# Kernel optimization log

Measured on AMD Instinct MI355X. Metric: run time of the kernel, lower is better.

Reference implementation:

```python
import jax, jax.numpy as jnp
import numpy as np

EPS_NORM = 1e-5
EPS_L2 = 1e-12
SCALE_VALUE = 50.0
FROM_VALUE = 0.4
VALUE_INTERVAL = 0.5


def mvn(x):
    # mean-variance norm per (b, c) over spatial dims; torch .var() is unbiased
    mean = jnp.mean(x, axis=(2, 3), keepdims=True)
    var = jnp.var(x, axis=(2, 3), keepdims=True, ddof=1)
    return (x - mean) / jnp.sqrt(var + EPS_NORM)


def conv1x1(x, W, b):
    # x: [b,c,h,w], W: [out,in], b: [out]
    return jnp.einsum('bchw,oc->bohw', x, W) + b[None, :, None, None]


def setup_inputs() -> dict:
    key = jax.random.key(0)
    ks = jax.random.split(key, 12)
    B, C, Hs, Ws = 4, 512, 64, 64
    HW = Hs * Ws  # 4096 == spatial_dims
    HID = HW // 16
    sc = 1.0 / np.sqrt(C)
    inp = {
        'content': jax.random.normal(ks[0], (B, C, Hs, Ws), jnp.float32),
        'style': jax.random.normal(ks[1], (B, C, Hs, Ws), jnp.float32),
        'Wf': jax.random.normal(ks[2], (C, C), jnp.float32) * sc,
        'bf': jnp.zeros((C,), jnp.float32),
        'Wg': jax.random.normal(ks[3], (C, C), jnp.float32) * sc,
        'bg': jnp.zeros((C,), jnp.float32),
        'Wh': jax.random.normal(ks[4], (C, C), jnp.float32) * sc,
        'bh': jnp.zeros((C,), jnp.float32),
        'Wout': jax.random.normal(ks[5], (C, C), jnp.float32) * sc,
        'bout': jnp.zeros((C,), jnp.float32),
        'W1': jax.random.normal(ks[6], (HID, HW), jnp.float32) * (1.0 / np.sqrt(HW)),
        'b1': jnp.zeros((HID,), jnp.float32),
        'W2': jax.random.normal(ks[7], (1, HID), jnp.float32) * (1.0 / np.sqrt(HID)),
        'b2': jnp.zeros((1,), jnp.float32),
    }
    return inp


def reference(content, style, Wf, bf, Wg, bg, Wh, bh, Wout, bout, W1, b1, W2, b2):
    B, C, H, W = content.shape
    HW = H * W

    Fq = conv1x1(mvn(content), Wf, bf).reshape(B, C, HW)   # query feats
    Gk = conv1x1(mvn(style), Wg, bg).reshape(B, C, HW)      # key feats
    Hv = conv1x1(style, Wh, bh).reshape(B, C, HW)           # value feats

    # affinity matrix: channel-L2-normalized cosine similarity [B, HW_c, HW_s]
    cf = content.reshape(B, C, HW)
    sf = style.reshape(B, C, HW)
    cf = cf / jnp.maximum(jnp.linalg.norm(cf, axis=1, keepdims=True), EPS_L2)
    sf = sf / jnp.maximum(jnp.linalg.norm(sf, axis=1, keepdims=True), EPS_L2)
    A = jnp.einsum('bck,bcl->bkl', cf, sf)

    # attention scores + softmax over style positions
    S = jax.nn.softmax(jnp.einsum('bck,bcl->bkl', Fq, Gk), axis=-1)

    # AEAModule: per-content-pixel adaptive clamp from affinity rows
    hmid = jnp.einsum('bkl,ol->bko', A, W1) + b1            # [B, HW, HID]
    hmid = jax.nn.leaky_relu(hmid, 0.2)
    psi = jax.nn.sigmoid(jnp.einsum('bko,po->bkp', hmid, W2) + b2)  # [B, HW, 1]
    clamp_value = psi * VALUE_INTERVAL + FROM_VALUE
    Sg = jax.nn.sigmoid(SCALE_VALUE * (S - clamp_value))    # gated attention

    # O = H @ Sg^T : [B, C, HW_c]
    O = jnp.einsum('bcl,bkl->bck', Hv, Sg).reshape(B, C, H, W)
    O = conv1x1(O, Wout, bout) + content
    return O
```

## Files before the change

### kernel.cpp

```cpp
#include <hip/hip_runtime.h>

typedef unsigned short u16;
typedef __attribute__((ext_vector_type(8))) short short8;
typedef __attribute__((ext_vector_type(4))) float f32x4;

static constexpr int Bn  = 4;
static constexpr int C   = 512;
static constexpr int HW  = 4096;
static constexpr int HID = 256;

__device__ __forceinline__ float bf2f(u16 u){
  union { unsigned int i; float f; } x; x.i = ((unsigned int)u) << 16; return x.f;
}
__device__ __forceinline__ u16 f2bf(float f){
  union { float f; unsigned int i; } x; x.f = f;
  return (u16)((x.i + 0x7fffu + ((x.i >> 16) & 1u)) >> 16);
}
__device__ __forceinline__ void gld16(const u16* g, u16* l){
  __builtin_amdgcn_global_load_lds((const __attribute__((address_space(1))) void*)g,
                                   (__attribute__((address_space(3))) void*)l, 16, 0, 0);
}

template<bool SPLIT>
__device__ __forceinline__ void mfma_core(const u16* __restrict__ Ah, const u16* __restrict__ Al, int pA,
                                          const u16* __restrict__ Bh, const u16* __restrict__ Bl, int pB,
                                          int K, u16* lds, f32x4 (&acc)[4][4]){
  const int tid  = threadIdx.x;
  const int lane = tid & 63, wave = tid >> 6;
  const int fr = lane & 15, kq = lane >> 4;
  const int wm = (wave & 1) * 64, wn = (wave >> 1) * 64;
  u16* As  = lds;
  u16* Bs  = lds + 4096;
  u16* As2 = SPLIT ? lds + 8192  : nullptr;
  u16* Bs2 = SPLIT ? lds + 12288 : nullptr;
  const int srow = wave*32 + (lane >> 2);
  const int sq   = (lane & 3) * 8;
  const size_t ga = (size_t)srow * pA + sq;
  const size_t gb = (size_t)srow * pB + sq;
  const int ldsc = wave * 1024;

  for (int k0 = 0; k0 < K; k0 += 32){
    __syncthreads();
    #pragma unroll
    for (int i = 0; i < 2; ++i){
      gld16(Ah + ga + (size_t)i*16*pA + k0, As + ldsc + i*512);
      gld16(Bh + gb + (size_t)i*16*pB + k0, Bs + ldsc + i*512);
      if (SPLIT){
        gld16(Al + ga + (size_t)i*16*pA + k0, As2 + ldsc + i*512);
        gld16(Bl + gb + (size_t)i*16*pB + k0, Bs2 + ldsc + i*512);
      }
    }
    __syncthreads();
    short8 a[4], b[4];
    #pragma unroll
    for (int i = 0; i < 4; ++i){
      a[i] = *(const short8*)&As[(wm + i*16 + fr)*32 + kq*8];
      b[i] = *(const short8*)&Bs[(wn + i*16 + fr)*32 + kq*8];
    }
    #pragma unroll
    for (int i = 0; i < 4; ++i)
      #pragma unroll
      for (int j = 0; j < 4; ++j)
        acc[i][j] = __builtin_amdgcn_mfma_f32_16x16x32_bf16(a[i], b[j], acc[i][j], 0, 0, 0);
    if (SPLIT){
      short8 a2[4], b2[4];
      #pragma unroll
      for (int i = 0; i < 4; ++i){
        a2[i] = *(const short8*)&As2[(wm + i*16 + fr)*32 + kq*8];
        b2[i] = *(const short8*)&Bs2[(wn + i*16 + fr)*32 + kq*8];
      }
      #pragma unroll
      for (int i = 0; i < 4; ++i)
        #pragma unroll
        for (int j = 0; j < 4; ++j){
          acc[i][j] = __builtin_amdgcn_mfma_f32_16x16x32_bf16(a[i],  b2[j], acc[i][j], 0, 0, 0);
          acc[i][j] = __builtin_amdgcn_mfma_f32_16x16x32_bf16(a2[i], b[j],  acc[i][j], 0, 0, 0);
        }
    }
  }
}

struct TileCtx { int wm, wn, cn, rq; };
__device__ __forceinline__ TileCtx tctx(){
  TileCtx t;
  const int wave = threadIdx.x >> 6, lane = threadIdx.x & 63;
  t.wm = blockIdx.y * 128 + (wave & 1) * 64;
  t.wn = blockIdx.x * 128 + (wave >> 1) * 64;
  t.cn = lane & 15; t.rq = (lane >> 4) * 4;
  return t;
}
#define ACC_ZERO(acc) { _Pragma("unroll") for (int i=0;i<4;++i) _Pragma("unroll") for (int j=0;j<4;++j) _Pragma("unroll") for (int r=0;r<4;++r) acc[i][j][r]=0.f; }

__global__ __launch_bounds__(256) void g_conv_split2(const u16* __restrict__ A0h, const u16* __restrict__ A0l,
                                                     const u16* __restrict__ A1h, const u16* __restrict__ A1l,
                                                     const u16* __restrict__ B0h, const u16* __restrict__ B0l,
                                                     const u16* __restrict__ B1h, const u16* __restrict__ B1l,
                                                     const float* __restrict__ bias0, const float* __restrict__ bias1,
                                                     u16* __restrict__ O0h, u16* __restrict__ O0l,
                                                     u16* __restrict__ O1h, u16* __restrict__ O1l,
                                                     size_t bsA, size_t bsO){
  __shared__ u16 lds[16384];
  const int zb = blockIdx.z, b = zb >> 1, z = zb & 1;
  const u16* Ah = (z ? A1h : A0h) + (size_t)b*bsA;  const u16* Al = (z ? A1l : A0l) + (size_t)b*bsA;
  const u16* Bh = z ? B1h : B0h;  const u16* Bl = z ? B1l : B0l;
  const float* bias = z ? bias1 : bias0;
  u16* Ohi = (z ? O1h : O0h) + (size_t)b*bsO;  u16* Olo = (z ? O1l : O0l) + (size_t)b*bsO;
  TileCtx t = tctx();
  f32x4 acc[4][4]; ACC_ZERO(acc);
  mfma_core<true>(Ah + (size_t)blockIdx.y*128*C, Al + (size_t)blockIdx.y*128*C, C,
                  Bh + (size_t)blockIdx.x*128*C, Bl + (size_t)blockIdx.x*128*C, C, C, lds, acc);
  #pragma unroll
  for (int fm = 0; fm < 4; ++fm)
    #pragma unroll
    for (int fn = 0; fn < 4; ++fn)
      #pragma unroll
      for (int r = 0; r < 4; ++r){
        int gm = t.wm + fm*16 + t.rq + r;
        int gn = t.wn + fn*16 + t.cn;
        float v = acc[fm][fn][r] + bias[gn];
        u16 h = f2bf(v);
        Ohi[(size_t)gm*C + gn] = h;
        Olo[(size_t)gm*C + gn] = f2bf(v - bf2f(h));
      }
}

__global__ __launch_bounds__(256) void g_gemm_split_f32(const u16* __restrict__ Ah, const u16* __restrict__ Al, int pA,
                                                        const u16* __restrict__ Bh, const u16* __restrict__ Bl, int pB,
                                                        int K, float* __restrict__ O, int pO,
                                                        size_t bsA, size_t bsB, size_t bsO){
  __shared__ u16 lds[16384];
  const int b = blockIdx.z;
  TileCtx t = tctx();
  f32x4 acc[4][4]; ACC_ZERO(acc);
  mfma_core<true>(Ah + (size_t)b*bsA + (size_t)blockIdx.y*128*pA,
                  Al + (size_t)b*bsA + (size_t)blockIdx.y*128*pA, pA,
                  Bh + (size_t)b*bsB + (size_t)blockIdx.x*128*pB,
                  Bl + (size_t)b*bsB + (size_t)blockIdx.x*128*pB, pB, K, lds, acc);
  float* Ob = O + (size_t)b*bsO;
  #pragma unroll
  for (int fm = 0; fm < 4; ++fm)
    #pragma unroll
    for (int fn = 0; fn < 4; ++fn)
      #pragma unroll
      for (int r = 0; r < 4; ++r)
        Ob[(size_t)(t.wm + fm*16 + t.rq + r)*pO + t.wn + fn*16 + t.cn] = acc[fm][fn][r];
}

__global__ __launch_bounds__(256) void g_gemm_biasm_bf16(const u16* __restrict__ A, int pA,
                                                         const u16* __restrict__ B, int pB,
                                                         int K, const float* __restrict__ bias,
                                                         u16* __restrict__ O, int pO,
                                                         size_t bsB, size_t bsO){
  __shared__ u16 lds[8192];
  const int b = blockIdx.z;
  TileCtx t = tctx();
  f32x4 acc[4][4]; ACC_ZERO(acc);
  mfma_core<false>(A + (size_t)blockIdx.y*128*pA, nullptr, pA,
                   B + (size_t)b*bsB + (size_t)blockIdx.x*128*pB, nullptr, pB, K, lds, acc);
  u16* Ob = O + (size_t)b*bsO;
  #pragma unroll
  for (int fm = 0; fm < 4; ++fm)
    #pragma unroll
    for (int fn = 0; fn < 4; ++fn)
      #pragma unroll
      for (int r = 0; r < 4; ++r){
        int gm = t.wm + fm*16 + t.rq + r;
        Ob[(size_t)gm*pO + t.wn + fn*16 + t.cn] = f2bf(acc[fm][fn][r] + bias[gm]);
      }
}

__global__ __launch_bounds__(256) void g_gemm_plain_bf16(const u16* __restrict__ A, int pA,
                                                         const u16* __restrict__ B, int pB,
                                                         int K, u16* __restrict__ O, int pO,
                                                         size_t bsA, size_t bsB, size_t bsO){
  __shared__ u16 lds[8192];
  const int b = blockIdx.z;
  TileCtx t = tctx();
  f32x4 acc[4][4]; ACC_ZERO(acc);
  mfma_core<false>(A + (size_t)b*bsA + (size_t)blockIdx.y*128*pA, nullptr, pA,
                   B + (size_t)b*bsB + (size_t)blockIdx.x*128*pB, nullptr, pB, K, lds, acc);
  u16* Ob = O + (size_t)b*bsO;
  #pragma unroll
  for (int fm = 0; fm < 4; ++fm)
    #pragma unroll
    for (int fn = 0; fn < 4; ++fn)
      #pragma unroll
      for (int r = 0; r < 4; ++r){
        int gm = t.wm + fm*16 + t.rq + r;
        Ob[(size_t)gm*pO + t.wn + fn*16 + t.cn] = f2bf(acc[fm][fn][r]);
      }
}

__global__ __launch_bounds__(256) void g_gemm_partial(const u16* __restrict__ A, int pA,
                                                      const u16* __restrict__ B, int pB,
                                                      int Kper, float* __restrict__ O, int pO,
                                                      size_t sliceStride, int slices,
                                                      size_t bsB, size_t bsO){
  __shared__ u16 lds[8192];
  const int zz = blockIdx.z;
  const int b = zz / slices, sl = zz - b*slices;
  TileCtx t = tctx();
  const int koff = sl * Kper;
  f32x4 acc[4][4]; ACC_ZERO(acc);
  mfma_core<false>(A + (size_t)blockIdx.y*128*pA + koff, nullptr, pA,
                   B + (size_t)b*bsB + (size_t)blockIdx.x*128*pB + koff, nullptr, pB, Kper, lds, acc);
  float* Oz = O + (size_t)b*bsO + (size_t)sl * sliceStride;
  #pragma unroll
  for (int fm = 0; fm < 4; ++fm)
    #pragma unroll
    for (int fn = 0; fn < 4; ++fn)
      #pragma unroll
      for (int r = 0; r < 4; ++r)
        Oz[(size_t)(t.wm + fm*16 + t.rq + r)*pO + t.wn + fn*16 + t.cn] = acc[fm][fn][r];
}

__global__ __launch_bounds__(256) void k_reduce(const float* __restrict__ in, size_t sliceStride,
                                                int S, u16* __restrict__ out,
                                                size_t bsIn, size_t bsOut){
  const int b = blockIdx.y;
  const float* inb = in + (size_t)b*bsIn;
  u16* outb = out + (size_t)b*bsOut;
  const size_t i4 = ((size_t)blockIdx.x*256 + threadIdx.x) * 4;
  float4 s = *(const float4*)&inb[i4];
  for (int z = 1; z < S; ++z){
    float4 v = *(const float4*)&inb[(size_t)z*sliceStride + i4];
    s.x += v.x; s.y += v.y; s.z += v.z; s.w += v.w;
  }
  u16 r0 = f2bf(s.x), r1 = f2bf(s.y), r2 = f2bf(s.z), r3 = f2bf(s.w);
  uint2 uo; uo.x = (unsigned)r0 | ((unsigned)r1 << 16);
  uo.y = (unsigned)r2 | ((unsigned)r3 << 16);
  *(uint2*)&outb[i4] = uo;
}

__global__ __launch_bounds__(256) void g_gemm_outconv(const u16* __restrict__ A, int pA,
                                                      const u16* __restrict__ B, int pB,
                                                      int K, const float* __restrict__ bias,
                                                      const float* __restrict__ res,
                                                      float* __restrict__ O,
                                                      size_t bsB, size_t bsRes, size_t bsO){
  __shared__ u16 lds[8192];
  const int b = blockIdx.z;
  TileCtx t = tctx();
  f32x4 acc[4][4]; ACC_ZERO(acc);
  mfma_core<false>(A + (size_t)blockIdx.y*128*pA, nullptr, pA,
                   B + (size_t)b*bsB + (size_t)blockIdx.x*128*pB, nullptr, pB, K, lds, acc);
  const float* resb = res + (size_t)b*bsRes;
  float* Ob = O + (size_t)b*bsO;
  #pragma unroll
  for (int fm = 0; fm < 4; ++fm)
    #pragma unroll
    for (int fn = 0; fn < 4; ++fn)
      #pragma unroll
      for (int r = 0; r < 4; ++r){
        int gm = t.wm + fm*16 + t.rq + r;
        int gn = t.wn + fn*16 + t.cn;
        Ob[(size_t)gm*HW + gn] = acc[fm][fn][r] + bias[gm] + resb[(size_t)gm*HW + gn];
      }
}

__global__ __launch_bounds__(256) void g_gemm_hmid(const u16* __restrict__ A, int pA,
                                                   const u16* __restrict__ B, int pB,
                                                   int K, const float* __restrict__ inc,
                                                   const float* __restrict__ b1,
                                                   float* __restrict__ O,
                                                   size_t bsA, size_t bsP, size_t bsInc, size_t bsO){
  __shared__ u16 lds[8192];
  const int b = blockIdx.z;
  TileCtx t = tctx();
  f32x4 acc[4][4]; ACC_ZERO(acc);
  mfma_core<false>(A + (size_t)b*bsA + (size_t)blockIdx.y*128*pA, nullptr, pA,
                   B + (size_t)b*bsP + (size_t)blockIdx.x*128*pB, nullptr, pB, K, lds, acc);
  const float* incb = inc + (size_t)b*bsInc;
  float* Ob = O + (size_t)b*bsO;
  #pragma unroll
  for (int fm = 0; fm < 4; ++fm)
    #pragma unroll
    for (int fn = 0; fn < 4; ++fn)
      #pragma unroll
      for (int r = 0; r < 4; ++r){
        int gm = t.wm + fm*16 + t.rq + r;
        int gn = t.wn + fn*16 + t.cn;
        float h = acc[fm][fn][r] * incb[gm] + b1[gn];
        Ob[(size_t)gm*HID + gn] = (h > 0.f) ? h : 0.2f*h;
      }
}

__global__ __launch_bounds__(256) void k_stats(const float* __restrict__ content,
                                               const float* __restrict__ style,
                                               float2* __restrict__ statsC,
                                               float2* __restrict__ statsS){
  const int bc = blockIdx.x;
  const float* X = (blockIdx.y == 0 ? content : style) + (size_t)bc * HW;
  float s = 0.f, sq = 0.f;
  for (int i = threadIdx.x; i < HW; i += 256){ float v = X[i]; s += v; sq += v*v; }
  __shared__ float rs[256], rq[256];
  rs[threadIdx.x] = s; rq[threadIdx.x] = sq; __syncthreads();
  for (int o = 128; o > 0; o >>= 1){
    if (threadIdx.x < o){ rs[threadIdx.x] += rs[threadIdx.x+o]; rq[threadIdx.x] += rq[threadIdx.x+o]; }
    __syncthreads();
  }
  if (threadIdx.x == 0){
    float mean = rs[0] / (float)HW;
    float var  = (rq[0] - rs[0]*mean) / (float)(HW - 1);
    (blockIdx.y == 0 ? statsC : statsS)[bc] = make_float2(mean, rsqrtf(var + 1e-5f));
  }
}

__global__ __launch_bounds__(256) void k_pixnorm(const float* __restrict__ content,
                                                 const float* __restrict__ style,
                                                 float* __restrict__ inc,
                                                 float* __restrict__ ins){
  const int b = blockIdx.y;
  const int k = blockIdx.x * 256 + threadIdx.x;
  const float* X = (blockIdx.z == 0 ? content : style) + (size_t)b * C * HW + k;
  float acc = 0.f;
  for (int c = 0; c < C; ++c){ float v = X[(size_t)c * HW]; acc += v*v; }
  (blockIdx.z == 0 ? inc : ins)[b*HW + k] = 1.f / fmaxf(sqrtf(acc), 1e-12f);
}

__global__ __launch_bounds__(256) void k_prep2(const float* __restrict__ Xc,
                                               const float* __restrict__ Xs,
                                               const float2* __restrict__ stC,
                                               const float2* __restrict__ stS,
                                               u16* __restrict__ ThiC, u16* __restrict__ TloC, u16* __restrict__ TrawC,
                                               u16* __restrict__ ThiS, u16* __restrict__ TloS, u16* __restrict__ TrawS,
                                               size_t bsX, size_t bsT, int bsSt){
  const int zb = blockIdx.z, b = zb >> 1, z = zb & 1;
  const float* X = (z ? Xs : Xc) + (size_t)b*bsX;
  const float2* stats = (z ? stS : stC) + (size_t)b*bsSt;
  u16* Thi = (z ? ThiS : ThiC) + (size_t)b*bsT;
  u16* Tlo = (z ? TloS : TloC) + (size_t)b*bsT;
  u16* Traw = (z ? TrawS : TrawC) + (size_t)b*bsT;
  __shared__ float tile[64][65];
  __shared__ float2 st[64];
  const int k0 = blockIdx.x*64, c0 = blockIdx.y*64;
  const int t = threadIdx.x;
  if (t < 64) st[t] = stats[c0 + t];
  const int j4 = (t & 15) * 4, i0 = t >> 4;
  for (int r = 0; r < 4; ++r){
    int i = i0 + r*16;
    float4 v = *(const float4*)&X[(size_t)(c0+i)*HW + k0 + j4];
    tile[i][j4+0] = v.x; tile[i][j4+1] = v.y; tile[i][j4+2] = v.z; tile[i][j4+3] = v.w;
  }
  __syncthreads();
  const int kk = t >> 2, cc = (t & 3) * 16;
  u16 h[16], l[16], rw[16];
  #pragma unroll
  for (int q = 0; q < 16; ++q){
    float x = tile[cc+q][kk];
    float2 s = st[cc+q];
    rw[q] = f2bf(x);
    float v = (x - s.x) * s.y;
    h[q] = f2bf(v);
    l[q] = f2bf(v - bf2f(h[q]));
  }
  size_t o = (size_t)(k0+kk)*C + c0 + cc;
  #pragma unroll
  for (int q = 0; q < 16; ++q){ Thi[o+q] = h[q]; Tlo[o+q] = l[q]; Traw[o+q] = rw[q]; }
}

__global__ __launch_bounds__(256) void k_scaleS(const float* __restrict__ style,
                                                const float* __restrict__ ins,
                                                u16* __restrict__ out,
                                                size_t bsS, size_t bsIns, size_t bsO){
  const int b = blockIdx.y;
  const size_t idx = ((size_t)blockIdx.x*256 + threadIdx.x) * 4;
  const int l = (int)(idx % HW);
  float4 v = *(const float4*)&style[(size_t)b*bsS + idx];
  float4 s = *(const float4*)&ins[(size_t)b*bsIns + l];
  u16* ob = out + (size_t)b*bsO;
  ob[idx+0] = f2bf(v.x*s.x); ob[idx+1] = f2bf(v.y*s.y);
  ob[idx+2] = f2bf(v.z*s.z); ob[idx+3] = f2bf(v.w*s.w);
}

__global__ __launch_bounds__(256) void k_wprep(const float* __restrict__ Wf, const float* __restrict__ Wg,
                                               const float* __restrict__ Wh, const float* __restrict__ Wo,
                                               const float* __restrict__ W1,
                                               u16* __restrict__ Wfh, u16* __restrict__ Wfl,
                                               u16* __restrict__ Wgh, u16* __restrict__ Wgl,
                                               u16* __restrict__ Whb, u16* __restrict__ Wob,
                                               u16* __restrict__ W1b){
  const int idx = (blockIdx.x*256 + threadIdx.x) * 4;
  const int mode = blockIdx.y;
  const int nsmall = C*C;
  if (mode == 4){
    float4 v = *(const float4*)&W1[idx];
    W1b[idx+0]=f2bf(v.x); W1b[idx+1]=f2bf(v.y); W1b[idx+2]=f2bf(v.z); W1b[idx+3]=f2bf(v.w);
    return;
  }
  if (idx >= nsmall) return;
  const float* src = (mode==0)?Wf:(mode==1)?Wg:(mode==2)?Wh:Wo;
  float4 v = *(const float4*)&src[idx];
  float vv[4] = {v.x, v.y, v.z, v.w};
  if (mode <= 1){
    u16* oh = (mode==0)?Wfh:Wgh;  u16* ol = (mode==0)?Wfl:Wgl;
    #pragma unroll
    for (int q = 0; q < 4; ++q){
      u16 hh = f2bf(vv[q]);
      oh[idx+q] = hh; ol[idx+q] = f2bf(vv[q] - bf2f(hh));
    }
  } else {
    u16* ob = (mode==2)?Whb:Wob;
    #pragma unroll
    for (int q = 0; q < 4; ++q) ob[idx+q] = f2bf(vv[q]);
  }
}

__global__ __launch_bounds__(256) void k_psi(const float* __restrict__ hmid,
                                             const float* __restrict__ W2,
                                             const float* __restrict__ b2,
                                             float* __restrict__ clampv,
                                             size_t bsH, size_t bsC){
  const int k = blockIdx.x, tid = threadIdx.x, b = blockIdx.y;
  __shared__ float red[256];
  red[tid] = hmid[(size_t)b*bsH + (size_t)k*HID + tid] * W2[tid];
  __syncthreads();
  for (int o = 128; o > 0; o >>= 1){
    if (tid < o) red[tid] += red[tid+o];
    __syncthreads();
  }
  if (tid == 0){
    float psi = 1.f/(1.f + expf(-(red[0] + b2[0])));
    clampv[(size_t)b*bsC + k] = psi*0.5f + 0.4f;
  }
}

__global__ __launch_bounds__(256) void k_softgate(float* __restrict__ T2,
                                                  const float* __restrict__ clampv,
                                                  size_t bsT, size_t bsC){
  const int k = blockIdx.x, tid = threadIdx.x, b = blockIdx.y;
  float* row = &T2[(size_t)b*bsT + (size_t)k*HW];
  float vals[16];
  float mx = -3.4e38f;
  #pragma unroll
  for (int i = 0; i < 16; ++i){ vals[i] = row[tid + i*256]; mx = fmaxf(mx, vals[i]); }
  __shared__ float red[256];
  red[tid] = mx; __syncthreads();
  for (int o = 128; o > 0; o >>= 1){
    if (tid < o) red[tid] = fmaxf(red[tid], red[tid+o]);
    __syncthreads();
  }
  mx = red[0]; __syncthreads();
  float s = 0.f;
  #pragma unroll
  for (int i = 0; i < 16; ++i){ vals[i] = expf(vals[i] - mx); s += vals[i]; }
  red[tid] = s; __syncthreads();
  for (int o = 128; o > 0; o >>= 1){
    if (tid < o) red[tid] += red[tid+o];
    __syncthreads();
  }
  const float inv = 1.f / red[0];
  const float cv = clampv[(size_t)b*bsC + k];
  u16* Sg = (u16*)row;
  #pragma unroll
  for (int i = 0; i < 16; ++i){
    float sg = 1.f/(1.f + expf(-50.f*(vals[i]*inv - cv)));
    Sg[tid + i*256] = f2bf(sg);
  }
}

extern "C" void kernel_launch(void* const* d_in, const int* in_sizes, int n_in,
                              void* d_out, int out_size, void* d_ws, size_t ws_size,
                              hipStream_t stream){
  const float* content = (const float*)d_in[0];
  const float* style   = (const float*)d_in[1];
  const float* Wf   = (const float*)d_in[2];  const float* bfv  = (const float*)d_in[3];
  const float* Wg   = (const float*)d_in[4];  const float* bg   = (const float*)d_in[5];
  const float* Wh   = (const float*)d_in[6];  const float* bh   = (const float*)d_in[7];
  const float* Wo   = (const float*)d_in[8];  const float* bout = (const float*)d_in[9];
  const float* W1   = (const float*)d_in[10]; const float* b1   = (const float*)d_in[11];
  const float* W2   = (const float*)d_in[12]; const float* b2   = (const float*)d_in[13];
  float* out = (float*)d_out;
  (void)in_sizes; (void)n_in; (void)out_size;

  char* ws = (char*)d_ws;
  size_t off = 0;
  auto alloc = [&](size_t bytes)->void*{
    void* p = (void*)(ws + off);
    off += (bytes + 255) & ~(size_t)255;
    return p;
  };
  float2* statsC = (float2*)alloc((size_t)Bn*C*sizeof(float2));
  float2* statsS = (float2*)alloc((size_t)Bn*C*sizeof(float2));
  float*  inc    = (float*) alloc((size_t)Bn*HW*sizeof(float));
  float*  ins    = (float*) alloc((size_t)Bn*HW*sizeof(float));
  float*  clampv = (float*) alloc((size_t)Bn*HW*sizeof(float));
  u16* Wfh = (u16*)alloc((size_t)C*C*2), *Wfl = (u16*)alloc((size_t)C*C*2);
  u16* Wgh = (u16*)alloc((size_t)C*C*2), *Wgl = (u16*)alloc((size_t)C*C*2);
  u16* Whb = (u16*)alloc((size_t)C*C*2), *Wob = (u16*)alloc((size_t)C*C*2);
  u16* W1b = (u16*)alloc((size_t)HID*HW*2);
  const size_t commonEnd = off;

  const size_t TPB = (size_t)HW*C;
  const size_t XB  = (size_t)C*HW;
  const size_t SLB = (size_t)Bn*TPB*2;

  k_stats  <<<dim3(Bn*C, 2),       256, 0, stream>>>(content, style, statsC, statsS);
  k_pixnorm<<<dim3(HW/256, Bn, 2), 256, 0, stream>>>(content, style, inc, ins);
  k_wprep  <<<dim3(HID*HW/1024, 5),256, 0, stream>>>(Wf, Wg, Wh, Wo, W1,
                                                     Wfh, Wfl, Wgh, Wgl, Whb, Wob, W1b);

  auto runPrep = [&](char* R, u16* bFqTh, u16* bFqTl, u16* bGkTh, u16* bGkTl,
                     u16* bHvb, u16* bPT){
    u16* bXcTh = (u16*)(R + 0*SLB);
    u16* bXcTl = (u16*)(R + 1*SLB);
    u16* bXsTh = (u16*)(R + 2*SLB);
    u16* bXsTl = (u16*)(R + 3*SLB);
    u16* bCrT  = (u16*)(R + 4*SLB);
    u16* bSrT  = (u16*)(R + 5*SLB);
    u16* bstS  = (u16*)(R + 6*SLB);
    float* bPpart = (float*)(R + 0*SLB);
    float* bhmid  = (float*)(R + 1*SLB);
    k_prep2 <<<dim3(HW/64, C/64, 2*Bn), 256, 0, stream>>>(content, style, statsC, statsS,
                                                          bXcTh, bXcTl, bCrT, bXsTh, bXsTl, bSrT,
                                                          XB, TPB, C);
    k_scaleS<<<dim3(C*HW/1024, Bn), 256, 0, stream>>>(style, ins, bstS, XB, HW, TPB);
    g_conv_split2<<<dim3(C/128, HW/128, 2*Bn), 256, 0, stream>>>(
        bXcTh, bXcTl, bXsTh, bXsTl, Wfh, Wfl, Wgh, Wgl, bfv, bg,
        bFqTh, bFqTl, bGkTh, bGkTl, TPB, TPB);
    g_gemm_biasm_bf16<<<dim3(HW/128, C/128, Bn), 256, 0, stream>>>(Whb, C, bSrT, C, C, bh,
                                                                   bHvb, HW, TPB, TPB);
    g_gemm_partial<<<dim3(C/128, HID/128, Bn*8), 256, 0, stream>>>(W1b, HW, bstS, HW, HW/8,
                                                                   bPpart, C, (size_t)HID*C, 8,
                                                                   TPB, (size_t)8*HID*C);
    k_reduce<<<dim3(HID*C/1024, Bn), 256, 0, stream>>>(bPpart, (size_t)HID*C, 8, bPT,
                                                       (size_t)8*HID*C, (size_t)HID*C);
    g_gemm_hmid<<<dim3(HID/128, HW/128, Bn), 256, 0, stream>>>(bCrT, C, bPT, C, C, inc, b1, bhmid,
                                                               TPB, (size_t)HID*C, HW, (size_t)HW*HID);
    k_psi<<<dim3(HW, Bn), 256, 0, stream>>>(bhmid, W2, b2, clampv, (size_t)HW*HID, HW);
  };

  {
    size_t o = commonEnd;
    auto al = [&](size_t bytes)->void*{ void* p = (void*)(ws + o); o += (bytes + 255) & ~(size_t)255; return p; };
    u16* bFqTh = (u16*)al(SLB), *bFqTl = (u16*)al(SLB);
    u16* bGkTh = (u16*)al(SLB), *bGkTl = (u16*)al(SLB);
    u16* bHvb  = (u16*)al(SLB);
    u16* bPT   = (u16*)al((size_t)Bn*HID*C*2);
    u16* bO1T  = (u16*)al(SLB);
    char* R    = (char*)al((size_t)Bn*HW*HW*4);
    if (o <= ws_size){
      runPrep(R, bFqTh, bFqTl, bGkTh, bGkTl, bHvb, bPT);
      float* bT2 = (float*)R;
      g_gemm_split_f32<<<dim3(HW/128, HW/128, Bn), 256, 0, stream>>>(bFqTh, bFqTl, C, bGkTh, bGkTl, C,
                                                                     C, bT2, HW,
                                                                     TPB, TPB, (size_t)HW*HW);
      k_softgate<<<dim3(HW, Bn), 256, 0, stream>>>(bT2, clampv, (size_t)HW*HW, HW);
      g_gemm_plain_bf16<<<dim3(C/128, HW/128, Bn), 256, 0, stream>>>((const u16*)bT2, 2*HW, bHvb, HW,
                                                                     HW, bO1T, C,
                                                                     (size_t)HW*HW*2, TPB, TPB);
      g_gemm_outconv<<<dim3(HW/128, C/128, Bn), 256, 0, stream>>>(Wob, C, bO1T, C, C, bout, content, out,
                                                                  TPB, XB, XB);
      return;
    }
  }

  {
    size_t o = commonEnd;
    auto al = [&](size_t bytes)->void*{ void* p = (void*)(ws + o); o += (bytes + 255) & ~(size_t)255; return p; };
    u16* bFqTh = (u16*)al(SLB), *bFqTl = (u16*)al(SLB);
    u16* bGkTh = (u16*)al(SLB), *bGkTl = (u16*)al(SLB);
    u16* bHvb  = (u16*)al(SLB);
    u16* bPT   = (u16*)al((size_t)Bn*HID*C*2);
    char* R    = (char*)al(7*SLB);
    if (o <= ws_size){
      runPrep(R, bFqTh, bFqTl, bGkTh, bGkTl, bHvb, bPT);
      float* T2s   = (float*)(R + 0*SLB);
      float* Opart = (float*)(R + 4*SLB);
      u16*   O1Ts  = (u16*)  (R + 6*SLB);
      for (int b = 0; b < Bn; ++b){
        g_gemm_split_f32<<<dim3(HW/128, HW/128), 256, 0, stream>>>(
            bFqTh + (size_t)b*TPB, bFqTl + (size_t)b*TPB, C,
            bGkTh + (size_t)b*TPB, bGkTl + (size_t)b*TPB, C, C, T2s, HW, 0, 0, 0);
        k_softgate<<<dim3(HW), 256, 0, stream>>>(T2s, clampv + (size_t)b*HW, 0, 0);
        g_gemm_partial<<<dim3(C/128, HW/128, 4), 256, 0, stream>>>(
            (const u16*)T2s, 2*HW, bHvb + (size_t)b*TPB, HW, 1024,
            Opart, C, (size_t)HW*C, 4, 0, 0);
        k_reduce<<<dim3(HW*C/1024), 256, 0, stream>>>(Opart, (size_t)HW*C, 4, O1Ts, 0, 0);
        g_gemm_outconv<<<dim3(HW/128, C/128), 256, 0, stream>>>(Wob, C, O1Ts, C, C, bout,
            content + (size_t)b*XB, out + (size_t)b*XB, 0, 0, 0);
      }
      return;
    }
  }

  off = commonEnd;
  u16* XcTh = (u16*)alloc((size_t)HW*C*2), *XcTl = (u16*)alloc((size_t)HW*C*2);
  u16* CrT  = (u16*)alloc((size_t)HW*C*2);
  u16* XsTh = (u16*)alloc((size_t)HW*C*2), *XsTl = (u16*)alloc((size_t)HW*C*2);
  u16* SrT  = (u16*)alloc((size_t)HW*C*2);
  u16* stS  = (u16*)alloc((size_t)C*HW*2);
  u16* FqTh = (u16*)alloc((size_t)HW*C*2), *FqTl = (u16*)alloc((size_t)HW*C*2);
  u16* GkTh = (u16*)alloc((size_t)HW*C*2), *GkTl = (u16*)alloc((size_t)HW*C*2);
  u16* Hvb  = (u16*)alloc((size_t)C*HW*2);
  u16* O1T  = (u16*)alloc((size_t)HW*C*2);
  u16* PT   = (u16*)alloc((size_t)HID*C*2);
  float* hmid  = (float*)alloc((size_t)HW*HID*sizeof(float));
  float* Ppart = (float*)alloc((size_t)16*HID*C*sizeof(float));
  float* Opart = (float*)alloc((size_t)4*HW*C*sizeof(float));
  float* T2    = (float*)alloc((size_t)HW*HW*sizeof(float));

  for (int b = 0; b < Bn; ++b){
    const float* cb = content + (size_t)b*C*HW;
    const float* sb = style   + (size_t)b*C*HW;
    const float* incb = inc + (size_t)b*HW;
    const float* insb = ins + (size_t)b*HW;
    float* clb = clampv + (size_t)b*HW;

    k_prep2 <<<dim3(HW/64, C/64, 2), 256, 0, stream>>>(cb, sb, statsC + (size_t)b*C, statsS + (size_t)b*C,
                                                       XcTh, XcTl, CrT, XsTh, XsTl, SrT, 0, 0, 0);
    k_scaleS<<<dim3(C*HW/1024),   256, 0, stream>>>(sb, insb, stS, 0, 0, 0);
    g_conv_split2<<<dim3(C/128, HW/128, 2), 256, 0, stream>>>(
        XcTh, XcTl, XsTh, XsTl, Wfh, Wfl, Wgh, Wgl, bfv, bg,
        FqTh, FqTl, GkTh, GkTl, 0, 0);
    g_gemm_biasm_bf16<<<dim3(HW/128, C/128), 256, 0, stream>>>(Whb, C, SrT, C, C, bh, Hvb, HW, 0, 0);
    g_gemm_partial<<<dim3(C/128, HID/128, 16), 256, 0, stream>>>(W1b, HW, stS, HW, 256,
                                                                 Ppart, C, (size_t)HID*C, 16, 0, 0);
    k_reduce<<<dim3(HID*C/1024), 256, 0, stream>>>(Ppart, (size_t)HID*C, 16, PT, 0, 0);
    g_gemm_hmid<<<dim3(HID/128, HW/128), 256, 0, stream>>>(CrT, C, PT, C, C, incb, b1, hmid, 0, 0, 0, 0);
    k_psi<<<dim3(HW), 256, 0, stream>>>(hmid, W2, b2, clb, 0, 0);
    g_gemm_split_f32<<<dim3(HW/128, HW/128), 256, 0, stream>>>(FqTh, FqTl, C, GkTh, GkTl, C, C, T2, HW, 0, 0, 0);
    k_softgate<<<dim3(HW), 256, 0, stream>>>(T2, clb, 0, 0);
    g_gemm_partial<<<dim3(C/128, HW/128, 4), 256, 0, stream>>>((const u16*)T2, 2*HW, Hvb, HW, 1024,
                                                               Opart, C, (size_t)HW*C, 4, 0, 0);
    k_reduce<<<dim3(HW*C/1024), 256, 0, stream>>>(Opart, (size_t)HW*C, 4, O1T, 0, 0);
    g_gemm_outconv<<<dim3(HW/128, C/128), 256, 0, stream>>>(Wob, C, O1T, C, C, bout, cb,
                                                            out + (size_t)b*C*HW, 0, 0, 0);
  }
}
```

Before: 914.6 us.

## Double-buffer LDS staging in MFMA GEMM core and fuse style scaling into prep

The shared GEMM core now uses two LDS buffers: global-to-LDS loads for the next K-slice are issued before computing the current one, with explicit vmcnt waits and barriers in place of the previous load-then-compute sequence. This aims to hide global load latency behind MFMA work across all GEMM kernels. LDS allocations double, which may lower occupancy for the split kernels (64KB per block). The separate k_scaleS kernel is also folded into k_prep2, which writes the scaled style output while it already holds the style tile, saving a launch and a second read of style.

```diff
diff --git a/kernel.cpp b/kernel.cpp
--- a/kernel.cpp
+++ b/kernel.cpp
@@ -29,45 +29,44 @@
   const int lane = tid & 63, wave = tid >> 6;
   const int fr = lane & 15, kq = lane >> 4;
   const int wm = (wave & 1) * 64, wn = (wave >> 1) * 64;
-  u16* As  = lds;
-  u16* Bs  = lds + 4096;
-  u16* As2 = SPLIT ? lds + 8192  : nullptr;
-  u16* Bs2 = SPLIT ? lds + 12288 : nullptr;
+  constexpr int HB = SPLIT ? 16384 : 8192;
   const int srow = wave*32 + (lane >> 2);
   const int sq   = (lane & 3) * 8;
   const size_t ga = (size_t)srow * pA + sq;
   const size_t gb = (size_t)srow * pB + sq;
   const int ldsc = wave * 1024;
 
-  for (int k0 = 0; k0 < K; k0 += 32){
-    __syncthreads();
+  auto stage = [&](int buf, int k0){
+    u16* L = lds + buf*HB;
     #pragma unroll
     for (int i = 0; i < 2; ++i){
-      gld16(Ah + ga + (size_t)i*16*pA + k0, As + ldsc + i*512);
-      gld16(Bh + gb + (size_t)i*16*pB + k0, Bs + ldsc + i*512);
-      if (SPLIT){
-        gld16(Al + ga + (size_t)i*16*pA + k0, As2 + ldsc + i*512);
-        gld16(Bl + gb + (size_t)i*16*pB + k0, Bs2 + ldsc + i*512);
+      gld16(Ah + ga + (size_t)i*16*pA + k0, L + ldsc + i*512);
+      gld16(Bh + gb + (size_t)i*16*pB + k0, L + 4096 + ldsc + i*512);
+      if constexpr (SPLIT){
+        gld16(Al + ga + (size_t)i*16*pA + k0, L + 8192  + ldsc + i*512);
+        gld16(Bl + gb + (size_t)i*16*pB + k0, L + 12288 + ldsc + i*512);
       }
     }
-    __syncthreads();
+  };
+  auto compute = [&](int buf){
+    u16* L = lds + buf*HB;
     short8 a[4], b[4];
     #pragma unroll
     for (int i = 0; i < 4; ++i){
-      a[i] = *(const short8*)&As[(wm + i*16 + fr)*32 + kq*8];
-      b[i] = *(const short8*)&Bs[(wn + i*16 + fr)*32 + kq*8];
+      a[i] = *(const short8*)&L[(wm + i*16 + fr)*32 + kq*8];
+      b[i] = *(const short8*)&L[4096 + (wn + i*16 + fr)*32 + kq*8];
     }
     #pragma unroll
     for (int i = 0; i < 4; ++i)
       #pragma unroll
       for (int j = 0; j < 4; ++j)
         acc[i][j] = __builtin_amdgcn_mfma_f32_16x16x32_bf16(a[i], b[j], acc[i][j], 0, 0, 0);
-    if (SPLIT){
+    if constexpr (SPLIT){
       short8 a2[4], b2[4];
       #pragma unroll
       for (int i = 0; i < 4; ++i){
-        a2[i] = *(const short8*)&As2[(wm + i*16 + fr)*32 + kq*8];
-        b2[i] = *(const short8*)&Bs2[(wn + i*16 + fr)*32 + kq*8];
+        a2[i] = *(const short8*)&L[8192  + (wm + i*16 + fr)*32 + kq*8];
+        b2[i] = *(const short8*)&L[12288 + (wn + i*16 + fr)*32 + kq*8];
       }
       #pragma unroll
       for (int i = 0; i < 4; ++i)
@@ -77,7 +76,22 @@
           acc[i][j] = __builtin_amdgcn_mfma_f32_16x16x32_bf16(a2[i], b[j],  acc[i][j], 0, 0, 0);
         }
     }
-  }
+  };
+
+  stage(0, 0);
+  int cur = 0;
+  for (int k0 = 32; k0 < K; k0 += 32){
+    stage(cur ^ 1, k0);
+    if constexpr (SPLIT) asm volatile("s_waitcnt vmcnt(8)" ::: "memory");
+    else                 asm volatile("s_waitcnt vmcnt(4)" ::: "memory");
+    __builtin_amdgcn_s_barrier();
+    compute(cur);
+    __builtin_amdgcn_s_barrier();
+    cur ^= 1;
+  }
+  asm volatile("s_waitcnt vmcnt(0)" ::: "memory");
+  __builtin_amdgcn_s_barrier();
+  compute(cur);
 }
 
 struct TileCtx { int wm, wn, cn, rq; };
@@ -99,7 +113,7 @@
                                                      u16* __restrict__ O0h, u16* __restrict__ O0l,
                                                      u16* __restrict__ O1h, u16* __restrict__ O1l,
                                                      size_t bsA, size_t bsO){
-  __shared__ u16 lds[16384];
+  __shared__ u16 lds[32768];
   const int zb = blockIdx.z, b = zb >> 1, z = zb & 1;
   const u16* Ah = (z ? A1h : A0h) + (size_t)b*bsA;  const u16* Al = (z ? A1l : A0l) + (size_t)b*bsA;
   const u16* Bh = z ? B1h : B0h;  const u16* Bl = z ? B1l : B0l;
@@ -128,7 +142,7 @@
                                                         const u16* __restrict__ Bh, const u16* __restrict__ Bl, int pB,
                                                         int K, float* __restrict__ O, int pO,
                                                         size_t bsA, size_t bsB, size_t bsO){
-  __shared__ u16 lds[16384];
+  __shared__ u16 lds[32768];
   const int b = blockIdx.z;
   TileCtx t = tctx();
   f32x4 acc[4][4]; ACC_ZERO(acc);
@@ -151,7 +165,7 @@
                                                          int K, const float* __restrict__ bias,
                                                          u16* __restrict__ O, int pO,
                                                          size_t bsB, size_t bsO){
-  __shared__ u16 lds[8192];
+  __shared__ u16 lds[16384];
   const int b = blockIdx.z;
   TileCtx t = tctx();
   f32x4 acc[4][4]; ACC_ZERO(acc);
@@ -173,7 +187,7 @@
                                                          const u16* __restrict__ B, int pB,
                                                          int K, u16* __restrict__ O, int pO,
                                                          size_t bsA, size_t bsB, size_t bsO){
-  __shared__ u16 lds[8192];
+  __shared__ u16 lds[16384];
   const int b = blockIdx.z;
   TileCtx t = tctx();
   f32x4 acc[4][4]; ACC_ZERO(acc);
@@ -196,7 +210,7 @@
                                                       int Kper, float* __restrict__ O, int pO,
                                                       size_t sliceStride, int slices,
                                                       size_t bsB, size_t bsO){
-  __shared__ u16 lds[8192];
+  __shared__ u16 lds[16384];
   const int zz = blockIdx.z;
   const int b = zz / slices, sl = zz - b*slices;
   TileCtx t = tctx();
@@ -238,7 +252,7 @@
                                                       const float* __restrict__ res,
                                                       float* __restrict__ O,
                                                       size_t bsB, size_t bsRes, size_t bsO){
-  __shared__ u16 lds[8192];
+  __shared__ u16 lds[16384];
   const int b = blockIdx.z;
   TileCtx t = tctx();
   f32x4 acc[4][4]; ACC_ZERO(acc);
@@ -264,7 +278,7 @@
                                                    const float* __restrict__ b1,
                                                    float* __restrict__ O,
                                                    size_t bsA, size_t bsP, size_t bsInc, size_t bsO){
-  __shared__ u16 lds[8192];
+  __shared__ u16 lds[16384];
   const int b = blockIdx.z;
   TileCtx t = tctx();
   f32x4 acc[4][4]; ACC_ZERO(acc);
@@ -321,26 +335,38 @@
 __global__ __launch_bounds__(256) void k_prep2(const float* __restrict__ Xc,
                                                const float* __restrict__ Xs,
                                                const float2* __restrict__ stC,
-                                               const float2* __restrict__ stS,
+                                               const float2* __restrict__ stSt,
+                                               const float* __restrict__ ins,
                                                u16* __restrict__ ThiC, u16* __restrict__ TloC, u16* __restrict__ TrawC,
                                                u16* __restrict__ ThiS, u16* __restrict__ TloS, u16* __restrict__ TrawS,
-                                               size_t bsX, size_t bsT, int bsSt){
+                                               u16* __restrict__ stSo,
+                                               size_t bsX, size_t bsT, int bsSt, size_t bsIns, size_t bsSo){
   const int zb = blockIdx.z, b = zb >> 1, z = zb & 1;
   const float* X = (z ? Xs : Xc) + (size_t)b*bsX;
-  const float2* stats = (z ? stS : stC) + (size_t)b*bsSt;
+  const float2* stats = (z ? stSt : stC) + (size_t)b*bsSt;
   u16* Thi = (z ? ThiS : ThiC) + (size_t)b*bsT;
   u16* Tlo = (z ? TloS : TloC) + (size_t)b*bsT;
   u16* Traw = (z ? TrawS : TrawC) + (size_t)b*bsT;
+  u16* sSb = stSo + (size_t)b*bsSo;
+  const float* insb = ins + (size_t)b*bsIns;
   __shared__ float tile[64][65];
   __shared__ float2 st[64];
   const int k0 = blockIdx.x*64, c0 = blockIdx.y*64;
   const int t = threadIdx.x;
   if (t < 64) st[t] = stats[c0 + t];
   const int j4 = (t & 15) * 4, i0 = t >> 4;
+  float4 sv;
+  if (z) sv = *(const float4*)&insb[k0 + j4];
   for (int r = 0; r < 4; ++r){
     int i = i0 + r*16;
     float4 v = *(const float4*)&X[(size_t)(c0+i)*HW + k0 + j4];
     tile[i][j4+0] = v.x; tile[i][j4+1] = v.y; tile[i][j4+2] = v.z; tile[i][j4+3] = v.w;
+    if (z){
+      u16 q0 = f2bf(v.x*sv.x), q1 = f2bf(v.y*sv.y), q2 = f2bf(v.z*sv.z), q3 = f2bf(v.w*sv.w);
+      uint2 uo; uo.x = (unsigned)q0 | ((unsigned)q1 << 16);
+      uo.y = (unsigned)q2 | ((unsigned)q3 << 16);
+      *(uint2*)&sSb[(size_t)(c0+i)*HW + k0 + j4] = uo;
+    }
   }
   __syncthreads();
   const int kk = t >> 2, cc = (t & 3) * 16;
@@ -357,20 +383,6 @@
   size_t o = (size_t)(k0+kk)*C + c0 + cc;
   #pragma unroll
   for (int q = 0; q < 16; ++q){ Thi[o+q] = h[q]; Tlo[o+q] = l[q]; Traw[o+q] = rw[q]; }
-}
-
-__global__ __launch_bounds__(256) void k_scaleS(const float* __restrict__ style,
-                                                const float* __restrict__ ins,
-                                                u16* __restrict__ out,
-                                                size_t bsS, size_t bsIns, size_t bsO){
-  const int b = blockIdx.y;
-  const size_t idx = ((size_t)blockIdx.x*256 + threadIdx.x) * 4;
-  const int l = (int)(idx % HW);
-  float4 v = *(const float4*)&style[(size_t)b*bsS + idx];
-  float4 s = *(const float4*)&ins[(size_t)b*bsIns + l];
-  u16* ob = out + (size_t)b*bsO;
-  ob[idx+0] = f2bf(v.x*s.x); ob[idx+1] = f2bf(v.y*s.y);
-  ob[idx+2] = f2bf(v.z*s.z); ob[idx+3] = f2bf(v.w*s.w);
 }
 
 __global__ __launch_bounds__(256) void k_wprep(const float* __restrict__ Wf, const float* __restrict__ Wg,
@@ -511,10 +523,9 @@
     u16* bstS  = (u16*)(R + 6*SLB);
     float* bPpart = (float*)(R + 0*SLB);
     float* bhmid  = (float*)(R + 1*SLB);
-    k_prep2 <<<dim3(HW/64, C/64, 2*Bn), 256, 0, stream>>>(content, style, statsC, statsS,
+    k_prep2 <<<dim3(HW/64, C/64, 2*Bn), 256, 0, stream>>>(content, style, statsC, statsS, ins,
                                                           bXcTh, bXcTl, bCrT, bXsTh, bXsTl, bSrT,
-                                                          XB, TPB, C);
-    k_scaleS<<<dim3(C*HW/1024, Bn), 256, 0, stream>>>(style, ins, bstS, XB, HW, TPB);
+                                                          bstS, XB, TPB, C, HW, TPB);
     g_conv_split2<<<dim3(C/128, HW/128, 2*Bn), 256, 0, stream>>>(
         bXcTh, bXcTl, bXsTh, bXsTl, Wfh, Wfl, Wgh, Wgl, bfv, bg,
         bFqTh, bFqTl, bGkTh, bGkTl, TPB, TPB);
@@ -608,8 +619,8 @@
     float* clb = clampv + (size_t)b*HW;
 
     k_prep2 <<<dim3(HW/64, C/64, 2), 256, 0, stream>>>(cb, sb, statsC + (size_t)b*C, statsS + (size_t)b*C,
-                                                       XcTh, XcTl, CrT, XsTh, XsTl, SrT, 0, 0, 0);
-    k_scaleS<<<dim3(C*HW/1024),   256, 0, stream>>>(sb, insb, stS, 0, 0, 0);
+                                                       insb, XcTh, XcTl, CrT, XsTh, XsTl, SrT,
+                                                       stS, 0, 0, 0, 0, 0);
     g_conv_split2<<<dim3(C/128, HW/128, 2), 256, 0, stream>>>(
         XcTh, XcTl, XsTh, XsTl, Wfh, Wfl, Wgh, Wgl, bfv, bg,
         FqTh, FqTl, GkTh, GkTl, 0, 0);
```

Result: slower. 934.6 us (+2.2%).
